# Kernel tuning notes

Hardware: AMD Instinct MI355X
Metric: run time of the kernel (lower is better)

## Reference

```python
import jax, jax.numpy as jnp
import numpy as np

SHAPE = (192, 224, 192)
COG = np.array([96.0, 112.0, 96.0], dtype=np.float32)


def _rotation(a):
    # a: (3,) angles. R = Rx @ Ry @ Rz, matching _compute_rotation.
    one = jnp.ones(()); zero = jnp.zeros(())
    cx, sx = jnp.cos(a[0]), jnp.sin(a[0])
    cy, sy = jnp.cos(a[1]), jnp.sin(a[1])
    cz, sz = jnp.cos(a[2]), jnp.sin(a[2])
    Rx = jnp.stack([jnp.stack([one, zero, zero]),
                    jnp.stack([zero, cx, -sx]),
                    jnp.stack([zero, sx, cx])])
    Ry = jnp.stack([jnp.stack([cy, zero, sy]),
                    jnp.stack([zero, one, zero]),
                    jnp.stack([-sy, zero, cy])])
    Rz = jnp.stack([jnp.stack([cz, -sz, zero]),
                    jnp.stack([sz, cz, zero]),
                    jnp.stack([zero, zero, one])])
    return Rx @ Ry @ Rz


def _compose_matrix(angle, translation, scaling, ref_v2r, flo_v2r):
    # factors are all 1; scaling param is log-scale -> exp
    ang = angle[0]
    sc = jnp.exp(scaling[0])
    tx = translation[0]
    eye = jnp.eye(4, dtype=angle.dtype)
    cog = jnp.asarray(COG, dtype=angle.dtype)
    T_center = eye.at[:3, 3].set(-cog)
    T_center_inv = eye.at[:3, 3].set(cog)
    T_sc = jnp.diag(jnp.concatenate([sc, jnp.ones((1,), angle.dtype)]))
    T_trans = eye.at[:3, 3].set(tx)
    T_rot = eye.at[:3, :3].set(_rotation(ang))
    T_rig = T_center_inv @ T_trans @ T_rot @ T_sc @ T_center
    return jnp.linalg.inv(flo_v2r) @ T_rig @ ref_v2r


def _trilinear(vol, di, dj, dk):
    # fast_3D_interp_torch, mode='linear': zero outside, clamp ceil at border
    D, H, W = vol.shape
    ok = (di > 0) & (dj > 0) & (dk > 0) & (di <= D - 1) & (dj <= H - 1) & (dk <= W - 1)
    fi = jnp.clip(jnp.floor(di), 0, D - 1)
    fj = jnp.clip(jnp.floor(dj), 0, H - 1)
    fk = jnp.clip(jnp.floor(dk), 0, W - 1)
    wi = di - fi; wj = dj - fj; wk = dk - fk
    fi = fi.astype(jnp.int32); fj = fj.astype(jnp.int32); fk = fk.astype(jnp.int32)
    ci = jnp.minimum(fi + 1, D - 1)
    cj = jnp.minimum(fj + 1, H - 1)
    ck = jnp.minimum(fk + 1, W - 1)
    c000 = vol[fi, fj, fk]; c100 = vol[ci, fj, fk]
    c010 = vol[fi, cj, fk]; c110 = vol[ci, cj, fk]
    c001 = vol[fi, fj, ck]; c101 = vol[ci, fj, ck]
    c011 = vol[fi, cj, ck]; c111 = vol[ci, cj, ck]
    out = ((c000 * (1 - wi) + c100 * wi) * (1 - wj) + (c010 * (1 - wi) + c110 * wi) * wj) * (1 - wk) \
        + ((c001 * (1 - wi) + c101 * wi) * (1 - wj) + (c011 * (1 - wi) + c111 * wi) * wj) * wk
    return jnp.where(ok, out, jnp.zeros((), vol.dtype))


def reference(image_targ, angle, translation, scaling, ref_v2r, flo_v2r):
    T = _compose_matrix(angle, translation, scaling, ref_v2r, flo_v2r)
    D, H, W = SHAPE
    ii, jj, kk = jnp.meshgrid(jnp.arange(D, dtype=image_targ.dtype),
                              jnp.arange(H, dtype=image_targ.dtype),
                              jnp.arange(W, dtype=image_targ.dtype), indexing='ij')
    di = T[0, 0] * ii + T[0, 1] * jj + T[0, 2] * kk + T[0, 3]
    dj = T[1, 0] * ii + T[1, 1] * jj + T[1, 2] * kk + T[1, 3]
    dk = T[2, 0] * ii + T[2, 1] * jj + T[2, 2] * kk + T[2, 3]
    out = _trilinear(image_targ[0, 0], di, dj, dk)
    return out[None, None]


def setup_inputs() -> dict:
    key = jax.random.key(0)
    k1, k2, k3, k4 = jax.random.split(key, 4)
    D, H, W = SHAPE
    image_targ = jax.random.normal(k1, (1, 1, D, H, W), dtype=jnp.float32)
    angle = jax.random.normal(k2, (1, 3), dtype=jnp.float32) * 0.05
    translation = jax.random.normal(k3, (1, 3), dtype=jnp.float32) * 2.0
    scaling = jax.random.normal(k4, (1, 3), dtype=jnp.float32) * 0.02
    ref_v2r = jnp.eye(4, dtype=jnp.float32)
    flo_v2r = jnp.eye(4, dtype=jnp.float32)
    return {"image_targ": image_targ, "angle": angle, "translation": translation,
            "scaling": scaling, "ref_v2r": ref_v2r, "flo_v2r": flo_v2r}
```

## Files before the change

### kernel.cpp

```cpp
#include <hip/hip_runtime.h>
#include <hip/hip_bf16.h>
#include <math.h>

#define D_DIM 192
#define H_DIM 224
#define W_DIM 192
#define TILE_ROWS 4
#define BLOCK 192
#define NUM_XCD 8


__device__ float g_T[12];

__device__ inline void mm4(const float* A, const float* B, float* C) {
#pragma unroll
    for (int r = 0; r < 4; ++r)
#pragma unroll
        for (int c = 0; c < 4; ++c) {
            float s = 0.f;
#pragma unroll
            for (int t = 0; t < 4; ++t) s += A[r * 4 + t] * B[t * 4 + c];
            C[r * 4 + c] = s;
        }
}

__device__ inline void inv4(const float* m, float* invOut) {
    float inv[16];
    inv[0]  =  m[5]*m[10]*m[15] - m[5]*m[11]*m[14] - m[9]*m[6]*m[15]
             + m[9]*m[7]*m[14] + m[13]*m[6]*m[11] - m[13]*m[7]*m[10];
    inv[4]  = -m[4]*m[10]*m[15] + m[4]*m[11]*m[14] + m[8]*m[6]*m[15]
             - m[8]*m[7]*m[14] - m[12]*m[6]*m[11] + m[12]*m[7]*m[10];
    inv[8]  =  m[4]*m[9]*m[15] - m[4]*m[11]*m[13] - m[8]*m[5]*m[15]
             + m[8]*m[7]*m[13] + m[12]*m[5]*m[11] - m[12]*m[7]*m[9];
    inv[12] = -m[4]*m[9]*m[14] + m[4]*m[10]*m[13] + m[8]*m[5]*m[14]
             - m[8]*m[6]*m[13] - m[12]*m[5]*m[10] + m[12]*m[6]*m[9];
    inv[1]  = -m[1]*m[10]*m[15] + m[1]*m[11]*m[14] + m[9]*m[2]*m[15]
             - m[9]*m[3]*m[14] - m[13]*m[2]*m[11] + m[13]*m[3]*m[10];
    inv[5]  =  m[0]*m[10]*m[15] - m[0]*m[11]*m[14] - m[8]*m[2]*m[15]
             + m[8]*m[3]*m[14] + m[12]*m[2]*m[11] - m[12]*m[3]*m[10];
    inv[9]  = -m[0]*m[9]*m[15] + m[0]*m[11]*m[13] + m[8]*m[1]*m[15]
             - m[8]*m[3]*m[13] - m[12]*m[1]*m[11] + m[12]*m[3]*m[9];
    inv[13] =  m[0]*m[9]*m[14] - m[0]*m[10]*m[13] - m[8]*m[1]*m[14]
             + m[8]*m[2]*m[13] + m[12]*m[1]*m[10] - m[12]*m[2]*m[9];
    inv[2]  =  m[1]*m[6]*m[15] - m[1]*m[7]*m[14] - m[5]*m[2]*m[15]
             + m[5]*m[3]*m[14] + m[13]*m[2]*m[7] - m[13]*m[3]*m[6];
    inv[6]  = -m[0]*m[6]*m[15] + m[0]*m[7]*m[14] + m[4]*m[2]*m[15]
             - m[4]*m[3]*m[14] - m[12]*m[2]*m[7] + m[12]*m[3]*m[6];
    inv[10] =  m[0]*m[5]*m[15] - m[0]*m[7]*m[13] - m[4]*m[1]*m[15]
             + m[4]*m[3]*m[13] + m[12]*m[1]*m[7] - m[12]*m[3]*m[5];
    inv[14] = -m[0]*m[5]*m[14] + m[0]*m[6]*m[13] + m[4]*m[1]*m[14]
             - m[4]*m[2]*m[13] - m[12]*m[1]*m[6] + m[12]*m[2]*m[5];
    inv[3]  = -m[1]*m[6]*m[11] + m[1]*m[7]*m[10] + m[5]*m[2]*m[11]
             - m[5]*m[3]*m[10] - m[9]*m[2]*m[7] + m[9]*m[3]*m[6];
    inv[7]  =  m[0]*m[6]*m[11] - m[0]*m[7]*m[10] - m[4]*m[2]*m[11]
             + m[4]*m[3]*m[10] + m[8]*m[2]*m[7] - m[8]*m[3]*m[6];
    inv[11] = -m[0]*m[5]*m[11] + m[0]*m[7]*m[9] + m[4]*m[1]*m[11]
             - m[4]*m[3]*m[9] - m[8]*m[1]*m[7] + m[8]*m[3]*m[5];
    inv[15] =  m[0]*m[5]*m[10] - m[0]*m[6]*m[9] - m[4]*m[1]*m[10]
             + m[4]*m[2]*m[9] + m[8]*m[1]*m[6] - m[8]*m[2]*m[5];

    float det = m[0]*inv[0] + m[1]*inv[4] + m[2]*inv[8] + m[3]*inv[12];
    det = 1.0f / det;
#pragma unroll
    for (int i = 0; i < 16; ++i) invOut[i] = inv[i] * det;
}

typedef float vf4 __attribute__((ext_vector_type(4)));

__global__ void compute_T_kernel(const float* __restrict__ ang,
                                 const float* __restrict__ tr,
                                 const float* __restrict__ scl,
                                 const float* __restrict__ ref_v2r,
                                 const float* __restrict__ flo_v2r) {
    if (threadIdx.x != 0 || blockIdx.x != 0) return;

    const float a0 = ang[0], a1 = ang[1], a2 = ang[2];
    const float tr0 = tr[0], tr1 = tr[1], tr2 = tr[2];
    const float sc0 = scl[0], sc1 = scl[1], sc2 = scl[2];
    vf4 refv[4], flov[4];
#pragma unroll
    for (int r = 0; r < 4; ++r) {
        refv[r] = *(const vf4*)(ref_v2r + 4 * r);
        flov[r] = *(const vf4*)(flo_v2r + 4 * r);
    }
    float refm[16], flom[16];
#pragma unroll
    for (int r = 0; r < 4; ++r)
#pragma unroll
        for (int c = 0; c < 4; ++c) {
            refm[r * 4 + c] = refv[r][c];
            flom[r * 4 + c] = flov[r][c];
        }

    const float cogx = 96.f, cogy = 112.f, cogz = 96.f;

    float cx = cosf(a0), sx = sinf(a0);
    float cy = cosf(a1), sy = sinf(a1);
    float cz = cosf(a2), sz = sinf(a2);

    float Rx[9] = {1, 0, 0, 0, cx, -sx, 0, sx, cx};
    float Ry[9] = {cy, 0, sy, 0, 1, 0, -sy, 0, cy};
    float Rz[9] = {cz, -sz, 0, sz, cz, 0, 0, 0, 1};
    float Ryz[9], R[9];
#pragma unroll
    for (int r = 0; r < 3; ++r)
#pragma unroll
        for (int c = 0; c < 3; ++c) {
            float s = 0.f;
#pragma unroll
            for (int t = 0; t < 3; ++t) s += Ry[r * 3 + t] * Rz[t * 3 + c];
            Ryz[r * 3 + c] = s;
        }
#pragma unroll
    for (int r = 0; r < 3; ++r)
#pragma unroll
        for (int c = 0; c < 3; ++c) {
            float s = 0.f;
#pragma unroll
            for (int t = 0; t < 3; ++t) s += Rx[r * 3 + t] * Ryz[t * 3 + c];
            R[r * 3 + c] = s;
        }

    float s0 = expf(sc0), s1 = expf(sc1), s2 = expf(sc2);

    float Tc[16]   = {1,0,0,-cogx, 0,1,0,-cogy, 0,0,1,-cogz, 0,0,0,1};
    float Tci[16]  = {1,0,0, cogx, 0,1,0, cogy, 0,0,1, cogz, 0,0,0,1};
    float Tsc[16]  = {s0,0,0,0, 0,s1,0,0, 0,0,s2,0, 0,0,0,1};
    float Ttr[16]  = {1,0,0,tr0, 0,1,0,tr1, 0,0,1,tr2, 0,0,0,1};
    float Trot[16] = {R[0],R[1],R[2],0, R[3],R[4],R[5],0, R[6],R[7],R[8],0, 0,0,0,1};

    float m1[16], m2[16], m3[16], Trig[16];
    mm4(Tci, Ttr, m1);
    mm4(m1, Trot, m2);
    mm4(m2, Tsc, m3);
    mm4(m3, Tc, Trig);

    float floinv[16], m4[16], T[16];
    inv4(flom, floinv);
    mm4(floinv, Trig, m4);
    mm4(m4, refm, T);

#pragma unroll
    for (int q = 0; q < 12; ++q) g_T[q] = T[q];
}


typedef float vf2 __attribute__((ext_vector_type(2)));

__global__ __launch_bounds__(BLOCK, 4) void resample_kernel(
    const float* __restrict__ vol,
    float* __restrict__ out) {

    constexpr int TILES_PER_I = H_DIM / TILE_ROWS;
    constexpr int NBLK = D_DIM * TILES_PER_I;
    constexpr int PER_XCD = NBLK / NUM_XCD;

    const int b = blockIdx.x;
    const int xcd = b & (NUM_XCD - 1);
    const int q = b >> 3;
    const int sb = xcd * PER_XCD + q;
    const int i = sb / TILES_PER_I;
    const int jbase = (sb - i * TILES_PER_I) * TILE_ROWS;
    const int k = threadIdx.x;

    const float t00 = g_T[0],  t01 = g_T[1],  t02 = g_T[2],  t03 = g_T[3];
    const float t10 = g_T[4],  t11 = g_T[5],  t12 = g_T[6],  t13 = g_T[7];
    const float t20 = g_T[8],  t21 = g_T[9],  t22 = g_T[10], t23 = g_T[11];

    const float fi = (float)i;
    const float fk = (float)k;

    vf2  p00[TILE_ROWS], p10[TILE_ROWS], p01[TILE_ROWS], p11[TILE_ROWS];
    float wi[TILE_ROWS], wj[TILE_ROWS], wk[TILE_ROWS];
    int   sel[TILE_ROWS];
    bool  okr[TILE_ROWS];

#pragma unroll
    for (int r = 0; r < TILE_ROWS; ++r) {
        const float fj = (float)(jbase + r);
        const float di = t00 * fi + t01 * fj + t02 * fk + t03;
        const float dj = t10 * fi + t11 * fj + t12 * fk + t13;
        const float dk = t20 * fi + t21 * fj + t22 * fk + t23;

        okr[r] = (di > 0.f) & (dj > 0.f) & (dk > 0.f) &
                 (di <= (float)(D_DIM - 1)) &
                 (dj <= (float)(H_DIM - 1)) &
                 (dk <= (float)(W_DIM - 1));

        float ffi = fminf(fmaxf(floorf(di), 0.f), (float)(D_DIM - 1));
        float ffj = fminf(fmaxf(floorf(dj), 0.f), (float)(H_DIM - 1));
        float ffk = fminf(fmaxf(floorf(dk), 0.f), (float)(W_DIM - 1));

        wi[r] = di - ffi; wj[r] = dj - ffj; wk[r] = dk - ffk;

        const int i0 = (int)ffi, j0 = (int)ffj, k0 = (int)ffk;
        const int i1 = min(i0 + 1, D_DIM - 1);
        const int j1 = min(j0 + 1, H_DIM - 1);
        const int koff = min(k0, W_DIM - 2);
        sel[r] = k0 - koff;

        const int base00 = (i0 * H_DIM + j0) * W_DIM + koff;
        const int base01 = (i0 * H_DIM + j1) * W_DIM + koff;
        const int base10 = (i1 * H_DIM + j0) * W_DIM + koff;
        const int base11 = (i1 * H_DIM + j1) * W_DIM + koff;

        p00[r] = *(const vf2*)(vol + base00);
        p10[r] = *(const vf2*)(vol + base10);
        p01[r] = *(const vf2*)(vol + base01);
        p11[r] = *(const vf2*)(vol + base11);
    }

    asm volatile(""
        : "+v"(p00[0]), "+v"(p10[0]), "+v"(p01[0]), "+v"(p11[0]),
          "+v"(p00[1]), "+v"(p10[1]), "+v"(p01[1]), "+v"(p11[1]),
          "+v"(p00[2]), "+v"(p10[2]), "+v"(p01[2]), "+v"(p11[2]),
          "+v"(p00[3]), "+v"(p10[3]), "+v"(p01[3]), "+v"(p11[3]));

#pragma unroll
    for (int r = 0; r < TILE_ROWS; ++r) {
        const float c000 = sel[r] ? p00[r].y : p00[r].x;
        const float c100 = sel[r] ? p10[r].y : p10[r].x;
        const float c010 = sel[r] ? p01[r].y : p01[r].x;
        const float c110 = sel[r] ? p11[r].y : p11[r].x;
        const float c001 = p00[r].y;
        const float c101 = p10[r].y;
        const float c011 = p01[r].y;
        const float c111 = p11[r].y;

        const float omwi = 1.f - wi[r], omwj = 1.f - wj[r], omwk = 1.f - wk[r];
        const float val = ((c000 * omwi + c100 * wi[r]) * omwj +
                           (c010 * omwi + c110 * wi[r]) * wj[r]) * omwk +
                          ((c001 * omwi + c101 * wi[r]) * omwj +
                           (c011 * omwi + c111 * wi[r]) * wj[r]) * wk[r];
        const float res = okr[r] ? val : 0.f;
        __builtin_nontemporal_store(res, &out[(i * H_DIM + (jbase + r)) * W_DIM + k]);
    }
}


extern "C" void kernel_launch(void* const* d_in, const int* in_sizes, int n_in,
                              void* d_out, int out_size, void* d_ws, size_t ws_size,
                              hipStream_t stream) {
    const float* image_targ  = (const float*)d_in[0];
    const float* angle       = (const float*)d_in[1];
    const float* translation = (const float*)d_in[2];
    const float* scaling     = (const float*)d_in[3];
    const float* ref_v2r     = (const float*)d_in[4];
    const float* flo_v2r     = (const float*)d_in[5];
    float* out = (float*)d_out;
    (void)d_ws; (void)ws_size;

    compute_T_kernel<<<1, 1, 0, stream>>>(angle, translation, scaling,
                                          ref_v2r, flo_v2r);

    const int nblk = D_DIM * (H_DIM / TILE_ROWS);
    resample_kernel<<<nblk, BLOCK, 0, stream>>>(image_targ, out);
}
```

Measured before the change: 114.4 us.

## Fuse transform computation into resample kernel and use persistent grid-stride blocks

Removes the separate single-thread kernel that builds the 3x4 transform. Each block now recomputes the matrix in thread 0, shares it through LDS, and broadcasts it with readfirstlane. The grid is capped at 2560 persistent blocks that loop over tiles within their XCD-assigned range, which amortises the per-block matrix setup. The aim is to drop one launch and the dependency gap between the two kernels, at the cost of redundant per-block trig and matrix work and a barrier.

```diff
diff --git a/kernel.cpp b/kernel.cpp
--- a/kernel.cpp
+++ b/kernel.cpp
@@ -1,5 +1,4 @@
 #include <hip/hip_runtime.h>
-#include <hip/hip_bf16.h>
 #include <math.h>
 
 #define D_DIM 192
@@ -8,9 +7,8 @@
 #define TILE_ROWS 4
 #define BLOCK 192
 #define NUM_XCD 8
-
-
-__device__ float g_T[12];
+#define PBLK 2560
+
 
 __device__ inline void mm4(const float* A, const float* B, float* C) {
 #pragma unroll
@@ -66,174 +64,185 @@
 }
 
 typedef float vf4 __attribute__((ext_vector_type(4)));
-
-__global__ void compute_T_kernel(const float* __restrict__ ang,
-                                 const float* __restrict__ tr,
-                                 const float* __restrict__ scl,
-                                 const float* __restrict__ ref_v2r,
-                                 const float* __restrict__ flo_v2r) {
-    if (threadIdx.x != 0 || blockIdx.x != 0) return;
-
-    const float a0 = ang[0], a1 = ang[1], a2 = ang[2];
-    const float tr0 = tr[0], tr1 = tr[1], tr2 = tr[2];
-    const float sc0 = scl[0], sc1 = scl[1], sc2 = scl[2];
-    vf4 refv[4], flov[4];
-#pragma unroll
-    for (int r = 0; r < 4; ++r) {
-        refv[r] = *(const vf4*)(ref_v2r + 4 * r);
-        flov[r] = *(const vf4*)(flo_v2r + 4 * r);
-    }
-    float refm[16], flom[16];
-#pragma unroll
-    for (int r = 0; r < 4; ++r)
-#pragma unroll
-        for (int c = 0; c < 4; ++c) {
-            refm[r * 4 + c] = refv[r][c];
-            flom[r * 4 + c] = flov[r][c];
-        }
-
-    const float cogx = 96.f, cogy = 112.f, cogz = 96.f;
-
-    float cx = cosf(a0), sx = sinf(a0);
-    float cy = cosf(a1), sy = sinf(a1);
-    float cz = cosf(a2), sz = sinf(a2);
-
-    float Rx[9] = {1, 0, 0, 0, cx, -sx, 0, sx, cx};
-    float Ry[9] = {cy, 0, sy, 0, 1, 0, -sy, 0, cy};
-    float Rz[9] = {cz, -sz, 0, sz, cz, 0, 0, 0, 1};
-    float Ryz[9], R[9];
-#pragma unroll
-    for (int r = 0; r < 3; ++r)
-#pragma unroll
-        for (int c = 0; c < 3; ++c) {
-            float s = 0.f;
-#pragma unroll
-            for (int t = 0; t < 3; ++t) s += Ry[r * 3 + t] * Rz[t * 3 + c];
-            Ryz[r * 3 + c] = s;
-        }
-#pragma unroll
-    for (int r = 0; r < 3; ++r)
-#pragma unroll
-        for (int c = 0; c < 3; ++c) {
-            float s = 0.f;
-#pragma unroll
-            for (int t = 0; t < 3; ++t) s += Rx[r * 3 + t] * Ryz[t * 3 + c];
-            R[r * 3 + c] = s;
-        }
-
-    float s0 = expf(sc0), s1 = expf(sc1), s2 = expf(sc2);
-
-    float Tc[16]   = {1,0,0,-cogx, 0,1,0,-cogy, 0,0,1,-cogz, 0,0,0,1};
-    float Tci[16]  = {1,0,0, cogx, 0,1,0, cogy, 0,0,1, cogz, 0,0,0,1};
-    float Tsc[16]  = {s0,0,0,0, 0,s1,0,0, 0,0,s2,0, 0,0,0,1};
-    float Ttr[16]  = {1,0,0,tr0, 0,1,0,tr1, 0,0,1,tr2, 0,0,0,1};
-    float Trot[16] = {R[0],R[1],R[2],0, R[3],R[4],R[5],0, R[6],R[7],R[8],0, 0,0,0,1};
-
-    float m1[16], m2[16], m3[16], Trig[16];
-    mm4(Tci, Ttr, m1);
-    mm4(m1, Trot, m2);
-    mm4(m2, Tsc, m3);
-    mm4(m3, Tc, Trig);
-
-    float floinv[16], m4[16], T[16];
-    inv4(flom, floinv);
-    mm4(floinv, Trig, m4);
-    mm4(m4, refm, T);
-
-#pragma unroll
-    for (int q = 0; q < 12; ++q) g_T[q] = T[q];
-}
-
-
 typedef float vf2 __attribute__((ext_vector_type(2)));
+
+__device__ inline float rfl(float x) {
+    return __int_as_float(__builtin_amdgcn_readfirstlane(__float_as_int(x)));
+}
 
 __global__ __launch_bounds__(BLOCK, 4) void resample_kernel(
     const float* __restrict__ vol,
+    const float* __restrict__ ang,
+    const float* __restrict__ tr,
+    const float* __restrict__ scl,
+    const float* __restrict__ ref_v2r,
+    const float* __restrict__ flo_v2r,
     float* __restrict__ out) {
 
     constexpr int TILES_PER_I = H_DIM / TILE_ROWS;
-    constexpr int NBLK = D_DIM * TILES_PER_I;
-    constexpr int PER_XCD = NBLK / NUM_XCD;
+    constexpr int NTILE_XCD = (D_DIM * TILES_PER_I) / NUM_XCD;
+    constexpr int BLK_XCD = PBLK / NUM_XCD;
+
+    __shared__ float sT[12];
+
+    if (threadIdx.x == 0) {
+        const float a0 = ang[0], a1 = ang[1], a2 = ang[2];
+        const float tr0 = tr[0], tr1 = tr[1], tr2 = tr[2];
+        const float sc0 = scl[0], sc1 = scl[1], sc2 = scl[2];
+        vf4 refv[4], flov[4];
+#pragma unroll
+        for (int r = 0; r < 4; ++r) {
+            refv[r] = *(const vf4*)(ref_v2r + 4 * r);
+            flov[r] = *(const vf4*)(flo_v2r + 4 * r);
+        }
+        float refm[16], flom[16];
+#pragma unroll
+        for (int r = 0; r < 4; ++r)
+#pragma unroll
+            for (int c = 0; c < 4; ++c) {
+                refm[r * 4 + c] = refv[r][c];
+                flom[r * 4 + c] = flov[r][c];
+            }
+
+        const float cogx = 96.f, cogy = 112.f, cogz = 96.f;
+        float cx = cosf(a0), sx = sinf(a0);
+        float cy = cosf(a1), sy = sinf(a1);
+        float cz = cosf(a2), sz = sinf(a2);
+
+        float Rx[9] = {1, 0, 0, 0, cx, -sx, 0, sx, cx};
+        float Ry[9] = {cy, 0, sy, 0, 1, 0, -sy, 0, cy};
+        float Rz[9] = {cz, -sz, 0, sz, cz, 0, 0, 0, 1};
+        float Ryz[9], R[9];
+#pragma unroll
+        for (int r = 0; r < 3; ++r)
+#pragma unroll
+            for (int c = 0; c < 3; ++c) {
+                float s = 0.f;
+#pragma unroll
+                for (int t = 0; t < 3; ++t) s += Ry[r * 3 + t] * Rz[t * 3 + c];
+                Ryz[r * 3 + c] = s;
+            }
+#pragma unroll
+        for (int r = 0; r < 3; ++r)
+#pragma unroll
+            for (int c = 0; c < 3; ++c) {
+                float s = 0.f;
+#pragma unroll
+                for (int t = 0; t < 3; ++t) s += Rx[r * 3 + t] * Ryz[t * 3 + c];
+                R[r * 3 + c] = s;
+            }
+
+        float s0 = expf(sc0), s1 = expf(sc1), s2 = expf(sc2);
+
+        float Tc[16]   = {1,0,0,-cogx, 0,1,0,-cogy, 0,0,1,-cogz, 0,0,0,1};
+        float Tci[16]  = {1,0,0, cogx, 0,1,0, cogy, 0,0,1, cogz, 0,0,0,1};
+        float Tsc[16]  = {s0,0,0,0, 0,s1,0,0, 0,0,s2,0, 0,0,0,1};
+        float Ttr[16]  = {1,0,0,tr0, 0,1,0,tr1, 0,0,1,tr2, 0,0,0,1};
+        float Trot[16] = {R[0],R[1],R[2],0, R[3],R[4],R[5],0,
+                          R[6],R[7],R[8],0, 0,0,0,1};
+
+        float m1[16], m2[16], m3[16], Trig[16];
+        mm4(Tci, Ttr, m1);
+        mm4(m1, Trot, m2);
+        mm4(m2, Tsc, m3);
+        mm4(m3, Tc, Trig);
+
+        float floinv[16], m4v[16], T[16];
+        inv4(flom, floinv);
+        mm4(floinv, Trig, m4v);
+        mm4(m4v, refm, T);
+
+#pragma unroll
+        for (int q = 0; q < 12; ++q) sT[q] = T[q];
+    }
+    __syncthreads();
+
+    const float t00 = rfl(sT[0]),  t01 = rfl(sT[1]);
+    const float t02 = rfl(sT[2]),  t03 = rfl(sT[3]);
+    const float t10 = rfl(sT[4]),  t11 = rfl(sT[5]);
+    const float t12 = rfl(sT[6]),  t13 = rfl(sT[7]);
+    const float t20 = rfl(sT[8]),  t21 = rfl(sT[9]);
+    const float t22 = rfl(sT[10]), t23 = rfl(sT[11]);
 
     const int b = blockIdx.x;
     const int xcd = b & (NUM_XCD - 1);
     const int q = b >> 3;
-    const int sb = xcd * PER_XCD + q;
-    const int i = sb / TILES_PER_I;
-    const int jbase = (sb - i * TILES_PER_I) * TILE_ROWS;
     const int k = threadIdx.x;
-
-    const float t00 = g_T[0],  t01 = g_T[1],  t02 = g_T[2],  t03 = g_T[3];
-    const float t10 = g_T[4],  t11 = g_T[5],  t12 = g_T[6],  t13 = g_T[7];
-    const float t20 = g_T[8],  t21 = g_T[9],  t22 = g_T[10], t23 = g_T[11];
-
-    const float fi = (float)i;
     const float fk = (float)k;
 
-    vf2  p00[TILE_ROWS], p10[TILE_ROWS], p01[TILE_ROWS], p11[TILE_ROWS];
-    float wi[TILE_ROWS], wj[TILE_ROWS], wk[TILE_ROWS];
-    int   sel[TILE_ROWS];
-    bool  okr[TILE_ROWS];
-
-#pragma unroll
-    for (int r = 0; r < TILE_ROWS; ++r) {
-        const float fj = (float)(jbase + r);
-        const float di = t00 * fi + t01 * fj + t02 * fk + t03;
-        const float dj = t10 * fi + t11 * fj + t12 * fk + t13;
-        const float dk = t20 * fi + t21 * fj + t22 * fk + t23;
-
-        okr[r] = (di > 0.f) & (dj > 0.f) & (dk > 0.f) &
-                 (di <= (float)(D_DIM - 1)) &
-                 (dj <= (float)(H_DIM - 1)) &
-                 (dk <= (float)(W_DIM - 1));
-
-        float ffi = fminf(fmaxf(floorf(di), 0.f), (float)(D_DIM - 1));
-        float ffj = fminf(fmaxf(floorf(dj), 0.f), (float)(H_DIM - 1));
-        float ffk = fminf(fmaxf(floorf(dk), 0.f), (float)(W_DIM - 1));
-
-        wi[r] = di - ffi; wj[r] = dj - ffj; wk[r] = dk - ffk;
-
-        const int i0 = (int)ffi, j0 = (int)ffj, k0 = (int)ffk;
-        const int i1 = min(i0 + 1, D_DIM - 1);
-        const int j1 = min(j0 + 1, H_DIM - 1);
-        const int koff = min(k0, W_DIM - 2);
-        sel[r] = k0 - koff;
-
-        const int base00 = (i0 * H_DIM + j0) * W_DIM + koff;
-        const int base01 = (i0 * H_DIM + j1) * W_DIM + koff;
-        const int base10 = (i1 * H_DIM + j0) * W_DIM + koff;
-        const int base11 = (i1 * H_DIM + j1) * W_DIM + koff;
-
-        p00[r] = *(const vf2*)(vol + base00);
-        p10[r] = *(const vf2*)(vol + base10);
-        p01[r] = *(const vf2*)(vol + base01);
-        p11[r] = *(const vf2*)(vol + base11);
-    }
-
-    asm volatile(""
-        : "+v"(p00[0]), "+v"(p10[0]), "+v"(p01[0]), "+v"(p11[0]),
-          "+v"(p00[1]), "+v"(p10[1]), "+v"(p01[1]), "+v"(p11[1]),
-          "+v"(p00[2]), "+v"(p10[2]), "+v"(p01[2]), "+v"(p11[2]),
-          "+v"(p00[3]), "+v"(p10[3]), "+v"(p01[3]), "+v"(p11[3]));
-
-#pragma unroll
-    for (int r = 0; r < TILE_ROWS; ++r) {
-        const float c000 = sel[r] ? p00[r].y : p00[r].x;
-        const float c100 = sel[r] ? p10[r].y : p10[r].x;
-        const float c010 = sel[r] ? p01[r].y : p01[r].x;
-        const float c110 = sel[r] ? p11[r].y : p11[r].x;
-        const float c001 = p00[r].y;
-        const float c101 = p10[r].y;
-        const float c011 = p01[r].y;
-        const float c111 = p11[r].y;
-
-        const float omwi = 1.f - wi[r], omwj = 1.f - wj[r], omwk = 1.f - wk[r];
-        const float val = ((c000 * omwi + c100 * wi[r]) * omwj +
-                           (c010 * omwi + c110 * wi[r]) * wj[r]) * omwk +
-                          ((c001 * omwi + c101 * wi[r]) * omwj +
-                           (c011 * omwi + c111 * wi[r]) * wj[r]) * wk[r];
-        const float res = okr[r] ? val : 0.f;
-        __builtin_nontemporal_store(res, &out[(i * H_DIM + (jbase + r)) * W_DIM + k]);
+    for (int qq = q; qq < NTILE_XCD; qq += BLK_XCD) {
+        const int sb = xcd * NTILE_XCD + qq;
+        const int i = sb / TILES_PER_I;
+        const int jbase = (sb - i * TILES_PER_I) * TILE_ROWS;
+        const float fi = (float)i;
+
+        vf2  p00[TILE_ROWS], p10[TILE_ROWS], p01[TILE_ROWS], p11[TILE_ROWS];
+        float wi[TILE_ROWS], wj[TILE_ROWS], wk[TILE_ROWS];
+        int   sel[TILE_ROWS];
+        bool  okr[TILE_ROWS];
+
+#pragma unroll
+        for (int r = 0; r < TILE_ROWS; ++r) {
+            const float fj = (float)(jbase + r);
+            const float di = t00 * fi + t01 * fj + t02 * fk + t03;
+            const float dj = t10 * fi + t11 * fj + t12 * fk + t13;
+            const float dk = t20 * fi + t21 * fj + t22 * fk + t23;
+
+            okr[r] = (di > 0.f) & (dj > 0.f) & (dk > 0.f) &
+                     (di <= (float)(D_DIM - 1)) &
+                     (dj <= (float)(H_DIM - 1)) &
+                     (dk <= (float)(W_DIM - 1));
+
+            float ffi = fminf(fmaxf(floorf(di), 0.f), (float)(D_DIM - 1));
+            float ffj = fminf(fmaxf(floorf(dj), 0.f), (float)(H_DIM - 1));
+            float ffk = fminf(fmaxf(floorf(dk), 0.f), (float)(W_DIM - 1));
+
+            wi[r] = di - ffi; wj[r] = dj - ffj; wk[r] = dk - ffk;
+
+            const int i0 = (int)ffi, j0 = (int)ffj, k0 = (int)ffk;
+            const int i1 = min(i0 + 1, D_DIM - 1);
+            const int j1 = min(j0 + 1, H_DIM - 1);
+            const int koff = min(k0, W_DIM - 2);
+            sel[r] = k0 - koff;
+
+            const int base00 = (i0 * H_DIM + j0) * W_DIM + koff;
+            const int base01 = (i0 * H_DIM + j1) * W_DIM + koff;
+            const int base10 = (i1 * H_DIM + j0) * W_DIM + koff;
+            const int base11 = (i1 * H_DIM + j1) * W_DIM + koff;
+
+            p00[r] = *(const vf2*)(vol + base00);
+            p10[r] = *(const vf2*)(vol + base10);
+            p01[r] = *(const vf2*)(vol + base01);
+            p11[r] = *(const vf2*)(vol + base11);
+        }
+
+        asm volatile(""
+            : "+v"(p00[0]), "+v"(p10[0]), "+v"(p01[0]), "+v"(p11[0]),
+              "+v"(p00[1]), "+v"(p10[1]), "+v"(p01[1]), "+v"(p11[1]),
+              "+v"(p00[2]), "+v"(p10[2]), "+v"(p01[2]), "+v"(p11[2]),
+              "+v"(p00[3]), "+v"(p10[3]), "+v"(p01[3]), "+v"(p11[3]));
+
+#pragma unroll
+        for (int r = 0; r < TILE_ROWS; ++r) {
+            const float c000 = sel[r] ? p00[r].y : p00[r].x;
+            const float c100 = sel[r] ? p10[r].y : p10[r].x;
+            const float c010 = sel[r] ? p01[r].y : p01[r].x;
+            const float c110 = sel[r] ? p11[r].y : p11[r].x;
+            const float c001 = p00[r].y;
+            const float c101 = p10[r].y;
+            const float c011 = p01[r].y;
+            const float c111 = p11[r].y;
+
+            const float omwi = 1.f - wi[r], omwj = 1.f - wj[r],
+                        omwk = 1.f - wk[r];
+            const float val = ((c000 * omwi + c100 * wi[r]) * omwj +
+                               (c010 * omwi + c110 * wi[r]) * wj[r]) * omwk +
+                              ((c001 * omwi + c101 * wi[r]) * omwj +
+                               (c011 * omwi + c111 * wi[r]) * wj[r]) * wk[r];
+            const float res = okr[r] ? val : 0.f;
+            __builtin_nontemporal_store(
+                res, &out[(i * H_DIM + (jbase + r)) * W_DIM + k]);
+        }
     }
 }
 
@@ -250,9 +259,6 @@
     float* out = (float*)d_out;
     (void)d_ws; (void)ws_size;
 
-    compute_T_kernel<<<1, 1, 0, stream>>>(angle, translation, scaling,
-                                          ref_v2r, flo_v2r);
-
-    const int nblk = D_DIM * (H_DIM / TILE_ROWS);
-    resample_kernel<<<nblk, BLOCK, 0, stream>>>(image_targ, out);
-}
+    resample_kernel<<<PBLK, BLOCK, 0, stream>>>(image_targ, angle, translation,
+                                                scaling, ref_v2r, flo_v2r, out);
+}
```

Measured after the change: 116.4 us. About the same (+1.7%).
